# Optimization experiments

Hardware: AMD Instinct MI355X
Metric: run time of the kernel (lower is better)

## Reference

```python
import jax, jax.numpy as jnp
import numpy as np

LN_EPS = 1e-5

def _ln(x, g, b):
    m = jnp.mean(x, axis=-1, keepdims=True)
    v = jnp.mean(jnp.square(x - m), axis=-1, keepdims=True)
    return (x - m) / jnp.sqrt(v + LN_EPS) * g + b

def setup_inputs() -> dict:
    key = jax.random.key(0)
    ks = jax.random.split(key, 24)
    B, S, N = 8, 4096, 32
    H = 32          # self_dim // 2
    D = 64          # self_dim
    O = 32          # output_dim
    def w(k, shape):
        fan_in = shape[0]
        return jax.random.normal(k, shape, dtype=jnp.float32) / np.sqrt(fan_in)
    inp = {
        "expr": jax.random.normal(ks[0], (B, S), dtype=jnp.float32),
        "neighbors": jax.random.normal(ks[1], (B, N, S), dtype=jnp.float32),
        "edge_info": jax.random.normal(ks[2], (B, S, N), dtype=jnp.float32),
        "mask": jax.random.bernoulli(ks[3], 0.1, (B, S)),
        # neighbors branch: Linear(2,H), LN(H), ReLU, Linear(H,H)
        "nW1": w(ks[4], (2, H)), "nb1": jnp.zeros((H,), jnp.float32),
        "nlg": jnp.ones((H,), jnp.float32), "nlb": jnp.zeros((H,), jnp.float32),
        "nW2": w(ks[5], (H, H)), "nb2": jnp.zeros((H,), jnp.float32),
        # self branch: Linear(1,H), LN(H), ReLU, Linear(H,H)
        "sW1": w(ks[6], (1, H)), "sb1": jnp.zeros((H,), jnp.float32),
        "slg": jnp.ones((H,), jnp.float32), "slb": jnp.zeros((H,), jnp.float32),
        "sW2": w(ks[7], (H, H)), "sb2": jnp.zeros((H,), jnp.float32),
        # shared: Linear(D,D), LN(D), ReLU, Linear(D,O)
        "hW1": w(ks[8], (D, D)), "hb1": jnp.zeros((D,), jnp.float32),
        "hlg": jnp.ones((D,), jnp.float32), "hlb": jnp.zeros((D,), jnp.float32),
        "hW2": w(ks[9], (D, O)), "hb2": jnp.zeros((O,), jnp.float32),
    }
    return inp

def reference(expr, neighbors, edge_info, mask,
              nW1, nb1, nlg, nlb, nW2, nb2,
              sW1, sb1, slg, slb, sW2, sb2,
              hW1, hb1, hlg, hlb, hW2, hb2):
    # neighbors: (B,N,S) -> (B,S,N); pair with edge_info -> (B,S,N,2)
    nfeat = jnp.stack([jnp.transpose(neighbors, (0, 2, 1)), edge_info], axis=-1)
    h = nfeat @ nW1 + nb1                      # (B,S,N,H)
    h = jax.nn.relu(_ln(h, nlg, nlb))
    h = h @ nW2 + nb2
    nagg = jnp.sum(h, axis=-2)                 # (B,S,H)
    # self branch
    e = expr[..., None]                        # (B,S,1)
    e = e @ sW1 + sb1                          # (B,S,H)
    e = jax.nn.relu(_ln(e, slg, slb))
    e = e @ sW2 + sb2
    # shared
    x = jnp.concatenate([e, nagg], axis=-1)    # (B,S,2H)
    x = x @ hW1 + hb1
    x = jax.nn.relu(_ln(x, hlg, hlb))
    x = x @ hW2 + hb2                          # (B,S,O)
    x = jnp.where(mask[..., None], 0.0, x)
    return x
```

## Files before the change

### kernel.cpp

```cpp
#include <hip/hip_runtime.h>
#include <hip/hip_bf16.h>


#define LN_EPS 1e-5f

__global__ __launch_bounds__(256) void gnn_fold(
    const float* __restrict__ nW1, const float* __restrict__ nb1,
    const float* __restrict__ nlg, const float* __restrict__ nlb,
    const float* __restrict__ nW2, const float* __restrict__ nb2,
    const float* __restrict__ sW1, const float* __restrict__ sb1,
    const float* __restrict__ slg, const float* __restrict__ slb,
    const float* __restrict__ sW2, const float* __restrict__ sb2,
    const float* __restrict__ hW1, const float* __restrict__ hb1,
    float* __restrict__ ws)
{
    int tid = blockIdx.x * 256 + threadIdx.x;
    int k = tid >> 6, m = tid & 63;
    float acc = 0.f;
    if (k < 32) {
        #pragma unroll 8
        for (int i = 0; i < 32; ++i) acc = fmaf(sW2[k*32 + i], hW1[i*64 + m], acc);
    } else {
        int kk = k - 32;
        #pragma unroll 8
        for (int i = 0; i < 32; ++i) acc = fmaf(nW2[kk*32 + i], hW1[(32 + i)*64 + m], acc);
    }
    ws[256 + k*64 + m] = acc;

    if (blockIdx.x == 0) {
        int t = threadIdx.x;
        if (t < 64) {
            float c = hb1[t];
            for (int i = 0; i < 32; ++i) {
                c = fmaf(sb2[i], hW1[i*64 + t], c);
                c = fmaf(32.f * nb2[i], hW1[(32 + i)*64 + t], c);
            }
            ws[4352 + t] = c;
        } else if (t < 96) {
            int j = t - 64;
            float m0 = 0.f, m1 = 0.f, mb = 0.f;
            for (int i = 0; i < 32; ++i) { m0 += nW1[i]; m1 += nW1[32 + i]; mb += nb1[i]; }
            m0 *= (1.f/32.f); m1 *= (1.f/32.f); mb *= (1.f/32.f);
            float a = nW1[j] - m0, c = nW1[32 + j] - m1, d = nb1[j] - mb;
            ws[j]       = a * nlg[j];
            ws[32 + j]  = c * nlg[j];
            ws[64 + j]  = d * nlg[j];
            ws[96 + j]  = nlb[j];
            float ms = 0.f, msb = 0.f;
            for (int i = 0; i < 32; ++i) { ms += sW1[i]; msb += sb1[i]; }
            ms *= (1.f/32.f); msb *= (1.f/32.f);
            float as = sW1[j] - ms, ds = sb1[j] - msb;
            ws[136 + j] = as * slg[j];
            ws[168 + j] = ds * slg[j];
            ws[200 + j] = slb[j];
        } else if (t == 96) {
            float m0 = 0.f, m1 = 0.f, mb = 0.f;
            for (int i = 0; i < 32; ++i) { m0 += nW1[i]; m1 += nW1[32 + i]; mb += nb1[i]; }
            m0 *= (1.f/32.f); m1 *= (1.f/32.f); mb *= (1.f/32.f);
            float qaa=0,qcc=0,qdd=0,qac=0,qad=0,qcd=0;
            for (int j = 0; j < 32; ++j) {
                float a = nW1[j] - m0, c = nW1[32 + j] - m1, d = nb1[j] - mb;
                qaa += a*a; qcc += c*c; qdd += d*d; qac += a*c; qad += a*d; qcd += c*d;
            }
            ws[128] = qaa*(1.f/32.f);
            ws[129] = qcc*(1.f/32.f);
            ws[130] = qdd*(1.f/32.f) + LN_EPS;
            ws[131] = 2.f*qac*(1.f/32.f);
            ws[132] = 2.f*qad*(1.f/32.f);
            ws[133] = 2.f*qcd*(1.f/32.f);
            float ms = 0.f, msb = 0.f;
            for (int i = 0; i < 32; ++i) { ms += sW1[i]; msb += sb1[i]; }
            ms *= (1.f/32.f); msb *= (1.f/32.f);
            float saa=0, sad=0, sdd=0;
            for (int j = 0; j < 32; ++j) {
                float as = sW1[j] - ms, ds = sb1[j] - msb;
                saa += as*as; sad += as*ds; sdd += ds*ds;
            }
            ws[232] = saa*(1.f/32.f);
            ws[233] = 2.f*sad*(1.f/32.f);
            ws[234] = sdd*(1.f/32.f) + LN_EPS;
        }
    }
}

__global__ __launch_bounds__(512, 4) void gnn_main(
    const float* __restrict__ expr, const float* __restrict__ neighbors,
    const float* __restrict__ edge_info, const int* __restrict__ mask,
    const float* __restrict__ hlg, const float* __restrict__ hlb,
    const float* __restrict__ hW2, const float* __restrict__ hb2,
    const float* __restrict__ ws, float* __restrict__ out)
{
    __shared__ float s_feat[64 * 33 * 2];
    __shared__ float s_X[64 * 65];
    __shared__ float s_red[64 * 17];
    __shared__ float s_expr[64];

    const int t  = threadIdx.x;
    const int g0 = blockIdx.x * 64;
    const int bb = g0 >> 12;
    const int s0 = g0 & 4095;
    const float* nbp = neighbors + ((size_t)bb * 32 * 4096 + s0);
    const float* eip = edge_info + (size_t)g0 * 32;

    {
        int n = t >> 4, c4 = t & 15;
        float4 v = *(const float4*)&nbp[n * 4096 + c4 * 4];
        int base = ((c4 * 4) * 33 + n) * 2;
        s_feat[base      ] = v.x;
        s_feat[base +  66] = v.y;
        s_feat[base + 132] = v.z;
        s_feat[base + 198] = v.w;
    }
    {
        int tk = t >> 3, n4 = t & 7;
        float4 v = *(const float4*)&eip[tk * 32 + n4 * 4];
        int base = (tk * 33 + n4 * 4) * 2 + 1;
        s_feat[base    ] = v.x;
        s_feat[base + 2] = v.y;
        s_feat[base + 4] = v.z;
        s_feat[base + 6] = v.w;
    }
    if (t < 64) s_expr[t] = expr[g0 + t];
    __syncthreads();

    const int tok = t >> 3;
    const int jb  = (t & 7) * 4;
    float Ag[4], Cg[4], Dg[4], lbv[4];
    *(float4*)Ag  = *(const float4*)&ws[jb];
    *(float4*)Cg  = *(const float4*)&ws[32 + jb];
    *(float4*)Dg  = *(const float4*)&ws[64 + jb];
    *(float4*)lbv = *(const float4*)&ws[96 + jb];
    const float qaa  = ws[128], qcc  = ws[129], qddp = ws[130];
    const float qac2 = ws[131], qad2 = ws[132], qcd2 = ws[133];

    float nsum[4] = {0.f, 0.f, 0.f, 0.f};
    #pragma unroll 8
    for (int n = 0; n < 32; ++n) {
        float2 f = *(const float2*)&s_feat[(tok * 33 + n) * 2];
        float v = fmaf(f.x, fmaf(qaa, f.x, qad2),
                  fmaf(f.y, fmaf(qcc, f.y, qcd2),
                  fmaf(qac2, f.x * f.y, qddp)));
        float inv = rsqrtf(v);
        #pragma unroll
        for (int i = 0; i < 4; ++i) {
            float r = fmaf(f.x, Ag[i], Dg[i]);
            r = fmaf(f.y, Cg[i], r);
            r = fmaf(r, inv, lbv[i]);
            nsum[i] += fmaxf(r, 0.f);
        }
    }

    {
        float ex = s_expr[tok];
        float As[4], Ds[4], sl[4];
        *(float4*)As = *(const float4*)&ws[136 + jb];
        *(float4*)Ds = *(const float4*)&ws[168 + jb];
        *(float4*)sl = *(const float4*)&ws[200 + jb];
        float vs   = fmaf(ex, fmaf(ws[232], ex, ws[233]), ws[234]);
        float invs = rsqrtf(vs);
        #pragma unroll
        for (int i = 0; i < 4; ++i) {
            float r = fmaf(ex, As[i], Ds[i]);
            r = fmaf(r, invs, sl[i]);
            s_X[tok * 65 + jb + i]      = fmaxf(r, 0.f);
            s_X[tok * 65 + 32 + jb + i] = nsum[i];
        }
    }
    __syncthreads();

    const int w = __builtin_amdgcn_readfirstlane(t >> 6);
    const int l = t & 63;
    const float* Gp = ws + 256 + w * 8;
    const float* cv = ws + 4352 + w * 8;
    float y[8];
    #pragma unroll
    for (int i = 0; i < 8; ++i) y[i] = cv[i];
    #pragma unroll 4
    for (int k = 0; k < 64; ++k) {
        float xk = s_X[l * 65 + k];
        const float* gk = Gp + k * 64;
        #pragma unroll
        for (int i = 0; i < 8; ++i) y[i] = fmaf(xk, gk[i], y[i]);
    }

    float sm = 0.f, s2 = 0.f;
    #pragma unroll
    for (int i = 0; i < 8; ++i) { sm += y[i]; s2 = fmaf(y[i], y[i], s2); }
    s_red[l * 17 + w * 2 + 0] = sm;
    s_red[l * 17 + w * 2 + 1] = s2;
    __syncthreads();
    float tot = 0.f, tot2 = 0.f;
    #pragma unroll
    for (int r = 0; r < 8; ++r) {
        tot  += s_red[l * 17 + r * 2 + 0];
        tot2 += s_red[l * 17 + r * 2 + 1];
    }
    float mean = tot * (1.f / 64.f);
    float var  = tot2 * (1.f / 64.f) - mean * mean;
    float linv = rsqrtf(var + LN_EPS);
    #pragma unroll
    for (int i = 0; i < 8; ++i) {
        float v = (y[i] - mean) * linv;
        v = fmaf(v, hlg[w * 8 + i], hlb[w * 8 + i]);
        s_X[l * 65 + w * 8 + i] = fmaxf(v, 0.f);
    }
    __syncthreads();

    const int ob = w * 4;
    int mk = mask[g0 + l];
    float o[4];
    #pragma unroll
    for (int i = 0; i < 4; ++i) o[i] = hb2[ob + i];
    #pragma unroll 4
    for (int m = 0; m < 64; ++m) {
        float ym = s_X[l * 65 + m];
        const float* h2 = hW2 + m * 32 + ob;
        #pragma unroll
        for (int i = 0; i < 4; ++i) o[i] = fmaf(ym, h2[i], o[i]);
    }
    float4 ov = make_float4(o[0], o[1], o[2], o[3]);
    if (mk) ov = make_float4(0.f, 0.f, 0.f, 0.f);
    *(float4*)(out + (size_t)(g0 + l) * 32 + ob) = ov;
}

extern "C" void kernel_launch(void* const* d_in, const int* in_sizes, int n_in,
                              void* d_out, int out_size, void* d_ws, size_t ws_size,
                              hipStream_t stream) {
    const float* expr      = (const float*)d_in[0];
    const float* neighbors = (const float*)d_in[1];
    const float* edge_info = (const float*)d_in[2];
    const int*   mask      = (const int*)d_in[3];
    const float* nW1 = (const float*)d_in[4];
    const float* nb1 = (const float*)d_in[5];
    const float* nlg = (const float*)d_in[6];
    const float* nlb = (const float*)d_in[7];
    const float* nW2 = (const float*)d_in[8];
    const float* nb2 = (const float*)d_in[9];
    const float* sW1 = (const float*)d_in[10];
    const float* sb1 = (const float*)d_in[11];
    const float* slg = (const float*)d_in[12];
    const float* slb = (const float*)d_in[13];
    const float* sW2 = (const float*)d_in[14];
    const float* sb2 = (const float*)d_in[15];
    const float* hW1 = (const float*)d_in[16];
    const float* hb1 = (const float*)d_in[17];
    const float* hlg = (const float*)d_in[18];
    const float* hlb = (const float*)d_in[19];
    const float* hW2 = (const float*)d_in[20];
    const float* hb2 = (const float*)d_in[21];
    float* ws  = (float*)d_ws;
    float* out = (float*)d_out;

    gnn_fold<<<16, 256, 0, stream>>>(nW1, nb1, nlg, nlb, nW2, nb2,
                                     sW1, sb1, slg, slb, sW2, sb2,
                                     hW1, hb1, ws);
    gnn_main<<<512, 512, 0, stream>>>(expr, neighbors, edge_info, mask,
                                      hlg, hlb, hW2, hb2, ws, out);
}
```

Measured before the change: 121.7 us.

## Fuse weight-folding kernel into main kernel and unfold W2·hW1 product

Removes the separate gnn_fold launch. Each block now recomputes the LayerNorm folding constants in shared memory using wave shuffle reductions. The pre-multiplied W2·hW1 matrix is dropped: each block applies sW2/nW2 to get an intermediate U (stored in the reused s_feat buffer), then applies hW1. This saves a kernel launch and its dependency, at the cost of an extra 64x32 matmul pass, an extra barrier and redundant per-block constant computation.

```diff
diff --git a/kernel.cpp b/kernel.cpp
--- a/kernel.cpp
+++ b/kernel.cpp
@@ -4,7 +4,15 @@
 
 #define LN_EPS 1e-5f
 
-__global__ __launch_bounds__(256) void gnn_fold(
+__device__ __forceinline__ float wsum64(float v) {
+    #pragma unroll
+    for (int m = 1; m < 64; m <<= 1) v += __shfl_xor(v, m);
+    return v;
+}
+
+__global__ __launch_bounds__(512, 4) void gnn_all(
+    const float* __restrict__ expr, const float* __restrict__ neighbors,
+    const float* __restrict__ edge_info, const int* __restrict__ mask,
     const float* __restrict__ nW1, const float* __restrict__ nb1,
     const float* __restrict__ nlg, const float* __restrict__ nlb,
     const float* __restrict__ nW2, const float* __restrict__ nb2,
@@ -12,88 +20,16 @@
     const float* __restrict__ slg, const float* __restrict__ slb,
     const float* __restrict__ sW2, const float* __restrict__ sb2,
     const float* __restrict__ hW1, const float* __restrict__ hb1,
-    float* __restrict__ ws)
-{
-    int tid = blockIdx.x * 256 + threadIdx.x;
-    int k = tid >> 6, m = tid & 63;
-    float acc = 0.f;
-    if (k < 32) {
-        #pragma unroll 8
-        for (int i = 0; i < 32; ++i) acc = fmaf(sW2[k*32 + i], hW1[i*64 + m], acc);
-    } else {
-        int kk = k - 32;
-        #pragma unroll 8
-        for (int i = 0; i < 32; ++i) acc = fmaf(nW2[kk*32 + i], hW1[(32 + i)*64 + m], acc);
-    }
-    ws[256 + k*64 + m] = acc;
-
-    if (blockIdx.x == 0) {
-        int t = threadIdx.x;
-        if (t < 64) {
-            float c = hb1[t];
-            for (int i = 0; i < 32; ++i) {
-                c = fmaf(sb2[i], hW1[i*64 + t], c);
-                c = fmaf(32.f * nb2[i], hW1[(32 + i)*64 + t], c);
-            }
-            ws[4352 + t] = c;
-        } else if (t < 96) {
-            int j = t - 64;
-            float m0 = 0.f, m1 = 0.f, mb = 0.f;
-            for (int i = 0; i < 32; ++i) { m0 += nW1[i]; m1 += nW1[32 + i]; mb += nb1[i]; }
-            m0 *= (1.f/32.f); m1 *= (1.f/32.f); mb *= (1.f/32.f);
-            float a = nW1[j] - m0, c = nW1[32 + j] - m1, d = nb1[j] - mb;
-            ws[j]       = a * nlg[j];
-            ws[32 + j]  = c * nlg[j];
-            ws[64 + j]  = d * nlg[j];
-            ws[96 + j]  = nlb[j];
-            float ms = 0.f, msb = 0.f;
-            for (int i = 0; i < 32; ++i) { ms += sW1[i]; msb += sb1[i]; }
-            ms *= (1.f/32.f); msb *= (1.f/32.f);
-            float as = sW1[j] - ms, ds = sb1[j] - msb;
-            ws[136 + j] = as * slg[j];
-            ws[168 + j] = ds * slg[j];
-            ws[200 + j] = slb[j];
-        } else if (t == 96) {
-            float m0 = 0.f, m1 = 0.f, mb = 0.f;
-            for (int i = 0; i < 32; ++i) { m0 += nW1[i]; m1 += nW1[32 + i]; mb += nb1[i]; }
-            m0 *= (1.f/32.f); m1 *= (1.f/32.f); mb *= (1.f/32.f);
-            float qaa=0,qcc=0,qdd=0,qac=0,qad=0,qcd=0;
-            for (int j = 0; j < 32; ++j) {
-                float a = nW1[j] - m0, c = nW1[32 + j] - m1, d = nb1[j] - mb;
-                qaa += a*a; qcc += c*c; qdd += d*d; qac += a*c; qad += a*d; qcd += c*d;
-            }
-            ws[128] = qaa*(1.f/32.f);
-            ws[129] = qcc*(1.f/32.f);
-            ws[130] = qdd*(1.f/32.f) + LN_EPS;
-            ws[131] = 2.f*qac*(1.f/32.f);
-            ws[132] = 2.f*qad*(1.f/32.f);
-            ws[133] = 2.f*qcd*(1.f/32.f);
-            float ms = 0.f, msb = 0.f;
-            for (int i = 0; i < 32; ++i) { ms += sW1[i]; msb += sb1[i]; }
-            ms *= (1.f/32.f); msb *= (1.f/32.f);
-            float saa=0, sad=0, sdd=0;
-            for (int j = 0; j < 32; ++j) {
-                float as = sW1[j] - ms, ds = sb1[j] - msb;
-                saa += as*as; sad += as*ds; sdd += ds*ds;
-            }
-            ws[232] = saa*(1.f/32.f);
-            ws[233] = 2.f*sad*(1.f/32.f);
-            ws[234] = sdd*(1.f/32.f) + LN_EPS;
-        }
-    }
-}
-
-__global__ __launch_bounds__(512, 4) void gnn_main(
-    const float* __restrict__ expr, const float* __restrict__ neighbors,
-    const float* __restrict__ edge_info, const int* __restrict__ mask,
     const float* __restrict__ hlg, const float* __restrict__ hlb,
     const float* __restrict__ hW2, const float* __restrict__ hb2,
-    const float* __restrict__ ws, float* __restrict__ out)
+    float* __restrict__ out)
 {
-    __shared__ float s_feat[64 * 33 * 2];
-    __shared__ float s_X[64 * 65];
-    __shared__ float s_red[64 * 17];
+    __shared__ __align__(16) float s_feat[64 * 33 * 2];
+    __shared__ __align__(16) float s_X[64 * 65];
+    __shared__ __align__(16) float s_red[64 * 17];
+    __shared__ __align__(16) float s_sm[240];
     __shared__ float s_expr[64];
+    float* s_U = s_feat;
 
     const int t  = threadIdx.x;
     const int g0 = blockIdx.x * 64;
@@ -120,18 +56,67 @@
         s_feat[base + 4] = v.z;
         s_feat[base + 6] = v.w;
     }
-    if (t < 64) s_expr[t] = expr[g0 + t];
+
+    if (t < 64) {
+        s_expr[t] = expr[g0 + t];
+        int j = t & 31;
+        bool lo = t < 32;
+        float w0 = lo ? nW1[j]      : 0.f;
+        float w1 = lo ? nW1[32 + j] : 0.f;
+        float b1 = lo ? nb1[j]      : 0.f;
+        float m0 = wsum64(w0) * (1.f/32.f);
+        float m1 = wsum64(w1) * (1.f/32.f);
+        float mb = wsum64(b1) * (1.f/32.f);
+        float a = w0 - m0, c = w1 - m1, d = b1 - mb;
+        float az = lo ? a : 0.f, cz = lo ? c : 0.f, dz = lo ? d : 0.f;
+        float qaa = wsum64(az * az) * (1.f/32.f);
+        float qcc = wsum64(cz * cz) * (1.f/32.f);
+        float qdd = wsum64(dz * dz) * (1.f/32.f);
+        float qac = wsum64(az * cz) * (2.f/32.f);
+        float qad = wsum64(az * dz) * (2.f/32.f);
+        float qcd = wsum64(cz * dz) * (2.f/32.f);
+        if (lo) {
+            float g = nlg[j];
+            s_sm[j]      = a * g;
+            s_sm[32 + j] = c * g;
+            s_sm[64 + j] = d * g;
+            s_sm[96 + j] = nlb[j];
+        }
+        if (t == 0) {
+            s_sm[224] = qaa; s_sm[225] = qcc; s_sm[226] = qdd + LN_EPS;
+            s_sm[227] = qac; s_sm[228] = qad; s_sm[229] = qcd;
+        }
+    } else if (t < 128) {
+        int j = (t - 64) & 31;
+        bool lo = t < 96;
+        float w0 = lo ? sW1[j] : 0.f;
+        float b0 = lo ? sb1[j] : 0.f;
+        float ms  = wsum64(w0) * (1.f/32.f);
+        float msb = wsum64(b0) * (1.f/32.f);
+        float a = w0 - ms, d = b0 - msb;
+        float az = lo ? a : 0.f, dz = lo ? d : 0.f;
+        float saa = wsum64(az * az) * (1.f/32.f);
+        float sad = wsum64(az * dz) * (2.f/32.f);
+        float sdd = wsum64(dz * dz) * (1.f/32.f);
+        if (lo) {
+            float g = slg[j];
+            s_sm[128 + j] = a * g;
+            s_sm[160 + j] = d * g;
+            s_sm[192 + j] = slb[j];
+        }
+        if (t == 96) { s_sm[230] = saa; s_sm[231] = sad; s_sm[232] = sdd + LN_EPS; }
+    }
     __syncthreads();
 
     const int tok = t >> 3;
     const int jb  = (t & 7) * 4;
     float Ag[4], Cg[4], Dg[4], lbv[4];
-    *(float4*)Ag  = *(const float4*)&ws[jb];
-    *(float4*)Cg  = *(const float4*)&ws[32 + jb];
-    *(float4*)Dg  = *(const float4*)&ws[64 + jb];
-    *(float4*)lbv = *(const float4*)&ws[96 + jb];
-    const float qaa  = ws[128], qcc  = ws[129], qddp = ws[130];
-    const float qac2 = ws[131], qad2 = ws[132], qcd2 = ws[133];
+    *(float4*)Ag  = *(const float4*)&s_sm[jb];
+    *(float4*)Cg  = *(const float4*)&s_sm[32 + jb];
+    *(float4*)Dg  = *(const float4*)&s_sm[64 + jb];
+    *(float4*)lbv = *(const float4*)&s_sm[96 + jb];
+    const float qaa  = s_sm[224], qcc  = s_sm[225], qddp = s_sm[226];
+    const float qac2 = s_sm[227], qad2 = s_sm[228], qcd2 = s_sm[229];
 
     float nsum[4] = {0.f, 0.f, 0.f, 0.f};
     #pragma unroll 8
@@ -153,10 +138,10 @@
     {
         float ex = s_expr[tok];
         float As[4], Ds[4], sl[4];
-        *(float4*)As = *(const float4*)&ws[136 + jb];
-        *(float4*)Ds = *(const float4*)&ws[168 + jb];
-        *(float4*)sl = *(const float4*)&ws[200 + jb];
-        float vs   = fmaf(ex, fmaf(ws[232], ex, ws[233]), ws[234]);
+        *(float4*)As = *(const float4*)&s_sm[128 + jb];
+        *(float4*)Ds = *(const float4*)&s_sm[160 + jb];
+        *(float4*)sl = *(const float4*)&s_sm[192 + jb];
+        float vs   = fmaf(ex, fmaf(s_sm[230], ex, s_sm[231]), s_sm[232]);
         float invs = rsqrtf(vs);
         #pragma unroll
         for (int i = 0; i < 4; ++i) {
@@ -170,17 +155,35 @@
 
     const int w = __builtin_amdgcn_readfirstlane(t >> 6);
     const int l = t & 63;
-    const float* Gp = ws + 256 + w * 8;
-    const float* cv = ws + 4352 + w * 8;
+    {
+        const float* W2  = (w < 4) ? sW2 : nW2;
+        const int   i0   = (w & 3) * 8;
+        const int   xoff = (w < 4) ? 0 : 32;
+        float u[8];
+        #pragma unroll
+        for (int i = 0; i < 8; ++i)
+            u[i] = (w < 4) ? sb2[i0 + i] : 32.f * nb2[i0 + i];
+        #pragma unroll 4
+        for (int k = 0; k < 32; ++k) {
+            float xk = s_X[l * 65 + xoff + k];
+            const float* wr = W2 + k * 32 + i0;
+            #pragma unroll
+            for (int i = 0; i < 8; ++i) u[i] = fmaf(xk, wr[i], u[i]);
+        }
+        #pragma unroll
+        for (int i = 0; i < 8; ++i) s_U[l * 65 + 8 * w + i] = u[i];
+    }
+    __syncthreads();
+
     float y[8];
     #pragma unroll
-    for (int i = 0; i < 8; ++i) y[i] = cv[i];
+    for (int i = 0; i < 8; ++i) y[i] = hb1[8 * w + i];
     #pragma unroll 4
     for (int k = 0; k < 64; ++k) {
-        float xk = s_X[l * 65 + k];
-        const float* gk = Gp + k * 64;
-        #pragma unroll
-        for (int i = 0; i < 8; ++i) y[i] = fmaf(xk, gk[i], y[i]);
+        float uk = s_U[l * 65 + k];
+        const float* hr = hW1 + k * 64 + 8 * w;
+        #pragma unroll
+        for (int i = 0; i < 8; ++i) y[i] = fmaf(uk, hr[i], y[i]);
     }
 
     float sm = 0.f, s2 = 0.f;
@@ -248,12 +251,10 @@
     const float* hlb = (const float*)d_in[19];
     const float* hW2 = (const float*)d_in[20];
     const float* hb2 = (const float*)d_in[21];
-    float* ws  = (float*)d_ws;
     float* out = (float*)d_out;
 
-    gnn_fold<<<16, 256, 0, stream>>>(nW1, nb1, nlg, nlb, nW2, nb2,
+    gnn_all<<<512, 512, 0, stream>>>(expr, neighbors, edge_info, mask,
+                                     nW1, nb1, nlg, nlb, nW2, nb2,
                                      sW1, sb1, slg, slb, sW2, sb2,
-                                     hW1, hb1, ws);
-    gnn_main<<<512, 512, 0, stream>>>(expr, neighbors, edge_info, mask,
-                                      hlg, hlb, hW2, hb2, ws, out);
+                                     hW1, hb1, hlg, hlb, hW2, hb2, out);
 }
```

Result: no change. 121.1 us (-0.5%).
